# Optimization experiments

Measured on AMD Instinct MI355X. Metric: run time of the kernel, lower is better.

The kernel has to match this reference:

```python
import jax, jax.numpy as jnp
import numpy as np

B, D, NR, H = 8, 64, 6, 3        # batch, input_dim, num_relation, num_hop
R2 = 2 * NR                      # relations incl. inverses
NUM_RULE = R2 ** H               # 1728 combinatorial rules
EPS = 1e-6
TAU = 1.0


def _rule_indices():
    # torch.meshgrid (indexing='ij') over num_hop copies of arange(2*NR), stacked on last dim
    a = np.arange(R2)
    grids = np.meshgrid(*([a] * H), indexing="ij")
    return jnp.asarray(np.stack(grids, -1).reshape(-1, H))  # [NUM_RULE, H] int


def setup_inputs() -> dict:
    key = jax.random.key(0)
    ks = jax.random.split(key, 11)
    s = 0.1
    return {
        "query": jax.random.normal(ks[0], (B, D), jnp.float32),
        "relation_emb": jax.random.normal(ks[1], (R2, D), jnp.float32) * s,      # nn.Embedding(2*NR, D)
        "indicator": jax.random.normal(ks[2], (D,), jnp.float32) * s,            # nn.Embedding(1, D)
        "rel_W": jax.random.normal(ks[3], (H, D, R2 * D), jnp.float32) * s,      # per-layer relation_linear
        "rel_b": jax.random.normal(ks[4], (H, R2 * D), jnp.float32) * s,
        "lin_W": jax.random.normal(ks[5], (H, 13 * D, D), jnp.float32) * s,      # per-layer combine Linear(13D->D)
        "lin_b": jax.random.normal(ks[6], (H, D), jnp.float32) * s,
        "mlp_W1": jax.random.normal(ks[7], (2 * D, D), jnp.float32) * s,
        "mlp_b1": jax.random.normal(ks[8], (D,), jnp.float32) * s,
        "mlp_W2": jax.random.normal(ks[9], (D, 1), jnp.float32) * s,
        "mlp_b2": jax.random.normal(ks[10], (1,), jnp.float32) * s,
    }


def reference(query, relation_emb, indicator, rel_W, rel_b, lin_W, lin_b,
              mlp_W1, mlp_b1, mlp_W2, mlp_b2):
    rel_idx = _rule_indices()                       # [R, H]
    Rn = rel_idx.shape[0]

    # PNA degree scales: each graph is a chain; degree_out+1 (boundary self-message)
    # node 0 -> 1 message (boundary only), nodes 1..H -> 2 messages (edge + boundary)
    log_deg_head = jnp.log(jnp.float32(1.0))
    log_deg_tail = jnp.log(jnp.float32(2.0))
    mean_scale = (log_deg_head + H * log_deg_tail) / (H + 1)
    s_head = log_deg_head / mean_scale
    s_tail = log_deg_tail / mean_scale
    scales_head = jnp.stack([jnp.float32(1.0), s_head, 1.0 / jnp.maximum(s_head, 1e-2)])
    scales_tail = jnp.stack([jnp.float32(1.0), s_tail, 1.0 / jnp.maximum(s_tail, 1e-2)])

    # node-0 PNA update: single message == boundary == indicator (constant across graphs)
    # stats layout per feature dim: (mean, max, min, std)
    f0 = jnp.stack([indicator, indicator, indicator,
                    jnp.full((D,), float(np.sqrt(EPS)), indicator.dtype)], -1).reshape(4 * D)
    upd0 = (f0[:, None] * scales_head).reshape(12 * D)

    # boundary / initial hidden: indicator at node 0 of every graph
    hidden = jnp.zeros((B, Rn, H + 1, D), query.dtype)
    hidden = hidden.at[:, :, 0, :].set(indicator)

    for l in range(H):
        # dependent relation table from the query (relation_linear)
        rel_table = (query @ rel_W[l] + rel_b[l]).reshape(B, R2, D)
        rel = rel_table[:, rel_idx]                 # [B, R, H, D] gather per edge
        msg = hidden[:, :, :-1, :] * rel            # distmult message on edges h -> h+1
        # tail-node PNA stats over message set {msg, boundary=0}
        mean = msg * 0.5
        mx = jnp.maximum(msg, 0.0)
        mn = jnp.minimum(msg, 0.0)
        std = jnp.sqrt(jnp.maximum(msg * msg * 0.25, EPS))   # sq_mean - mean^2 = msg^2/4
        feats = jnp.stack([mean, mx, mn, std], -1).reshape(B, Rn, H, 4 * D)
        upd_tail = (feats[..., None] * scales_tail).reshape(B, Rn, H, 12 * D)
        upd = jnp.concatenate(
            [jnp.broadcast_to(upd0, (B, Rn, 1, 12 * D)), upd_tail], axis=2)
        # combine: relu(Linear(cat([input, update])))
        hidden = jax.nn.relu(
            jnp.concatenate([hidden, upd], -1) @ lin_W[l] + lin_b[l])

    # readout at tail node H, concat per-node query
    feat = jnp.concatenate(
        [hidden[:, :, H, :], jnp.broadcast_to(query[:, None, :], (B, Rn, D))], -1)
    score = (jax.nn.relu(feat @ mlp_W1 + mlp_b1) @ mlp_W2 + mlp_b2)[..., 0]   # [B, R]
    attention = jax.nn.softmax(score / TAU, axis=-1)
    r_emb = relation_emb[rel_idx]                   # [R, H, D]
    subgoals = jnp.einsum("br,rhd->bhd", attention, r_emb)
    masks = jnp.ones((B, H), bool)
    return subgoals, masks
```

## Files before the change

### kernel.cpp

```cpp
#include <hip/hip_runtime.h>
#include <hip/hip_bf16.h>


typedef const float* fp;

#define WS_WT     0
#define WS_RELT   49152
#define WS_QW1    67584
#define WS_Q2     68096
#define WS_QW3    141824
#define WS_SCORES 142592

__device__ __forceinline__ void acc4f(float q, float rv, float4 wv, float& acc){
  float m  = q*rv;
  float am = fabsf(m);
  acc += m  * wv.x;
  acc += am * wv.y;
  acc += fmaxf(am, 2e-3f) * wv.z;
}

__global__ void k_pre1(fp lin_W, fp query, fp rel_W, fp rel_b, fp mlp_W1,
                       fp mlp_b1, float* ws){
  int t = blockIdx.x*256 + threadIdx.x;
  if (t < 49152){
    int c = t & 3; int j = (t>>2)&63; int d = (t>>8)&63; int l = t>>14;
    fp W = lin_W + (size_t)l*832*64 + (64 + 12*d)*64 + j;
    float v = 0.f;
    if (c == 0){
      float w0 = W[0]   + (4.f/3.f)*W[64]  + 0.75f*W[128];
      float w1 = W[192] + (4.f/3.f)*W[256] + 0.75f*W[320];
      float w2 = W[384] + (4.f/3.f)*W[448] + 0.75f*W[512];
      v = 0.5f*w0 + 0.5f*(w1 + w2);
    } else if (c == 1){
      float w1 = W[192] + (4.f/3.f)*W[256] + 0.75f*W[320];
      float w2 = W[384] + (4.f/3.f)*W[448] + 0.75f*W[512];
      v = 0.5f*(w1 - w2);
    } else if (c == 2){
      v = 0.5f*(W[576] + (4.f/3.f)*W[640] + 0.75f*W[704]);
    }
    ws[WS_WT + t] = v;
  } else if (t < 67584){
    int e = t - 49152;
    int d = e & 63; int j = (e>>6)%12; int b = (e/768)&7; int l = e/6144;
    float acc = rel_b[l*768 + j*64 + d];
    fp W = rel_W + (size_t)l*64*768 + j*64 + d;
    fp q = query + b*64;
    #pragma unroll 8
    for (int k=0;k<64;k++) acc += q[k] * W[k*768];
    ws[WS_RELT + e] = acc;
  } else if (t < 68096){
    int e = t - 67584; int b = e>>6; int j = e&63;
    float acc = mlp_b1[j];
    fp q = query + b*64;
    #pragma unroll 8
    for (int i=0;i<64;i++) acc += q[i] * mlp_W1[(64+i)*64 + j];
    ws[WS_QW1 + e] = acc;
  }
}

__global__ void k_mid(fp indicator, fp lin_W, fp lin_b, float* ws){
  __shared__ float sC2[64], sC2W[64], sP1[64], sQ3[12][64];
  int tid = threadIdx.x;
  int w = tid>>6, j = tid&63;
  bool isQ2 = blockIdx.x < 96;
  int b  = isQ2 ? blockIdx.x/12 : blockIdx.x-96;
  int i0 = isQ2 ? blockIdx.x%12 : 0;
  if (w == 0){
    float acc = lin_b[j];
    #pragma unroll 8
    for (int d=0; d<64; d++) acc += 2e-3f * ws[WS_WT + ((d<<6)+j)*4 + 2];
    sC2[j] = fmaxf(acc, 0.f);
  } else if (w == 1 && isQ2){
    const float4* W4 = (const float4*)(ws + WS_WT);
    const float* rel = ws + WS_RELT + (b*12+i0)*64;
    float acc = lin_b[j];
    #pragma unroll 4
    for (int d=0; d<64; d++) acc4f(indicator[d], rel[d], W4[(d<<6)+j], acc);
    sP1[j] = fmaxf(acc, 0.f);
  }
  __syncthreads();
  if (w == 0){
    float a2 = lin_b[64+j];
    fp W1 = lin_W + 832*64;
    #pragma unroll 8
    for (int k=0;k<64;k++) a2 += sC2[k] * W1[k*64+j];
    sC2W[j] = a2;
  }
  __syncthreads();
  const float4* W4 = (const float4*)(ws + WS_WT + 16384);
  const float* rel = ws + WS_RELT + 6144 + (b*12+w)*64;
  if (isQ2){
    float acc = sC2W[j];
    #pragma unroll 4
    for (int d=0; d<64; d++) acc4f(sP1[d], rel[d], W4[(d<<6)+j], acc);
    ws[WS_Q2 + ((b*12+i0)*12+w)*64 + j] = fmaxf(acc, 0.f);
  } else {
    float acc = sC2W[j];
    #pragma unroll 4
    for (int d=0; d<64; d++) acc4f(sC2[d], rel[d], W4[(d<<6)+j], acc);
    sQ3[w][j] = fmaxf(acc, 0.f);
    __syncthreads();
    fp W2 = lin_W + 2*832*64;
    float a = lin_b[128+j];
    #pragma unroll 8
    for (int k=0;k<64;k++) a += sQ3[w][k]*W2[k*64+j];
    ws[WS_QW3 + (b*12+w)*64 + j] = a;
  }
}

__global__ __launch_bounds__(256) void k_score(fp mlp_W1, fp mlp_W2, float* ws){
  __shared__ float wt_s[4096];
  __shared__ float fin[4][4][64];
  int tid = threadIdx.x, w = tid>>6, j = tid&63;
  int wave = blockIdx.x*4 + w;
  int b = blockIdx.x/108;
  int rem = wave%432;
  int i0 = rem/36; int t36 = rem%36;
  int i2 = t36/3;  int i1b = (t36%3)*4;
  const float4* relv = (const float4*)(ws + WS_RELT + 12288 + (b*12+i2)*64);
  const float* q2base = ws + WS_Q2 + ((b*12+i0)*12 + i1b)*64;
  const float4* q0v = (const float4*)(q2base);
  const float4* q1v = (const float4*)(q2base + 64);
  const float4* q2v = (const float4*)(q2base + 128);
  const float4* q3v = (const float4*)(q2base + 192);
  float a0 = ws[WS_QW3 + (b*12+i2)*64 + j];
  float acc0=a0, acc1=a0, acc2=a0, acc3=a0;
  const float4* Wt2 = (const float4*)(ws + WS_WT + 32768);
  for (int ch=0; ch<4; ch++){
    __syncthreads();
    {
      const float4* src = Wt2 + ch*1024;
      float4* dst = (float4*)wt_s;
      #pragma unroll
      for (int k=0; k<4; k++) dst[tid + k*256] = src[tid + k*256];
    }
    __syncthreads();
    #pragma unroll
    for (int dq=0; dq<4; dq++){
      int dc = ch*4 + dq;
      float4 rv = relv[dc];
      float4 qa = q0v[dc], qb = q1v[dc], qc = q2v[dc], qd = q3v[dc];
      const float4* wl = (const float4*)wt_s + dq*256 + j;
      float4 w0 = wl[0], w1 = wl[64], w2 = wl[128], w3 = wl[192];
      acc4f(qa.x, rv.x, w0, acc0); acc4f(qb.x, rv.x, w0, acc1);
      acc4f(qc.x, rv.x, w0, acc2); acc4f(qd.x, rv.x, w0, acc3);
      acc4f(qa.y, rv.y, w1, acc0); acc4f(qb.y, rv.y, w1, acc1);
      acc4f(qc.y, rv.y, w1, acc2); acc4f(qd.y, rv.y, w1, acc3);
      acc4f(qa.z, rv.z, w2, acc0); acc4f(qb.z, rv.z, w2, acc1);
      acc4f(qc.z, rv.z, w2, acc2); acc4f(qd.z, rv.z, w2, acc3);
      acc4f(qa.w, rv.w, w3, acc0); acc4f(qb.w, rv.w, w3, acc1);
      acc4f(qc.w, rv.w, w3, acc2); acc4f(qd.w, rv.w, w3, acc3);
    }
  }
  __syncthreads();
  fin[w][0][j]=fmaxf(acc0,0.f); fin[w][1][j]=fmaxf(acc1,0.f);
  fin[w][2][j]=fmaxf(acc2,0.f); fin[w][3][j]=fmaxf(acc3,0.f);
  __syncthreads();
  float qw = ws[WS_QW1 + b*64 + j];
  float w2v = mlp_W2[j];
  float h0=qw, h1=qw, h2=qw, h3=qw;
  #pragma unroll 8
  for (int i=0;i<64;i++){
    float wv = mlp_W1[i*64+j];
    h0 += fin[w][0][i]*wv; h1 += fin[w][1][i]*wv;
    h2 += fin[w][2][i]*wv; h3 += fin[w][3][i]*wv;
  }
  float s0=fmaxf(h0,0.f)*w2v, s1=fmaxf(h1,0.f)*w2v;
  float s2=fmaxf(h2,0.f)*w2v, s3=fmaxf(h3,0.f)*w2v;
  #pragma unroll
  for (int off=32; off>0; off>>=1){
    s0 += __shfl_down(s0, off, 64); s1 += __shfl_down(s1, off, 64);
    s2 += __shfl_down(s2, off, 64); s3 += __shfl_down(s3, off, 64);
  }
  if (j == 0){
    int rbase = i0*144 + i1b*12 + i2;
    float* S = ws + WS_SCORES + b*1728 + rbase;
    S[0] = s0; S[12] = s1; S[24] = s2; S[36] = s3;
  }
}

__global__ void k_final(fp relation_emb, float* ws, float* out){
  int b = blockIdx.x, tid = threadIdx.x;
  __shared__ float se[1728];
  __shared__ float red[256];
  __shared__ float pb[36][4];
  __shared__ float bins[36];
  const float* sc = ws + WS_SCORES + b*1728;
  float mx = -1e30f;
  for (int r=tid; r<1728; r+=256){ float v = sc[r]; se[r] = v; mx = fmaxf(mx, v); }
  red[tid] = mx; __syncthreads();
  for (int s=128; s>0; s>>=1){ if (tid<s) red[tid] = fmaxf(red[tid], red[tid+s]); __syncthreads(); }
  mx = red[0]; __syncthreads();
  float ts = 0.f;
  for (int r=tid; r<1728; r+=256){ float e = __expf(se[r]-mx); se[r] = e; ts += e; }
  red[tid] = ts; __syncthreads();
  for (int s=128; s>0; s>>=1){ if (tid<s) red[tid] += red[tid+s]; __syncthreads(); }
  float tot = red[0]; __syncthreads();
  if (tid < 144){
    int bin = tid>>2, q = tid&3;
    int h = bin/12, jj = bin%12;
    float a = 0.f;
    if (h == 0){
      const float* p = se + jj*144 + q*36;
      #pragma unroll 4
      for (int k=0;k<36;k++) a += p[k];
    } else if (h == 1){
      for (int t=q*36; t<q*36+36; t++) a += se[(t/12)*144 + jj*12 + (t%12)];
    } else {
      for (int t=q*36; t<q*36+36; t++) a += se[(t/12)*144 + (t%12)*12 + jj];
    }
    pb[bin][q] = a;
  }
  __syncthreads();
  if (tid < 36) bins[tid] = (pb[tid][0]+pb[tid][1]) + (pb[tid][2]+pb[tid][3]);
  __syncthreads();
  if (tid < 192){
    int h = tid>>6, d = tid&63;
    float acc = 0.f;
    #pragma unroll
    for (int jj=0; jj<12; jj++) acc += bins[h*12+jj] * relation_emb[jj*64+d];
    out[b*192 + tid] = acc/tot;
  }
  if (tid >= 192 && tid < 195){
    out[1536 + b*3 + (tid-192)] = 1.0f;
  }
}

extern "C" void kernel_launch(void* const* d_in, const int* in_sizes, int n_in,
                              void* d_out, int out_size, void* d_ws, size_t ws_size,
                              hipStream_t stream){
  fp query        = (fp)d_in[0];
  fp relation_emb = (fp)d_in[1];
  fp indicator    = (fp)d_in[2];
  fp rel_W        = (fp)d_in[3];
  fp rel_b        = (fp)d_in[4];
  fp lin_W        = (fp)d_in[5];
  fp lin_b        = (fp)d_in[6];
  fp mlp_W1       = (fp)d_in[7];
  fp mlp_b1       = (fp)d_in[8];
  fp mlp_W2       = (fp)d_in[9];
  float* ws = (float*)d_ws;
  float* out = (float*)d_out;

  k_pre1 <<<266, 256, 0, stream>>>(lin_W, query, rel_W, rel_b, mlp_W1, mlp_b1, ws);
  k_mid  <<<104, 768, 0, stream>>>(indicator, lin_W, lin_b, ws);
  k_score<<<864, 256, 0, stream>>>(mlp_W1, mlp_W2, ws);
  k_final<<<8,   256, 0, stream>>>(relation_emb, ws, out);
}
```

Measured before the change: 119.4 us.

## Precompute message products and clamps in shared memory, use wave-shuffle softmax reductions

The per-element products q*rel and their clamped absolute values are now computed once into shared memory instead of being recomputed inside every weight-accumulation loop in k_mid and k_score. The inner loops then read float4 vectors of the precomputed values. The k_final max and sum reductions switch from a shared-memory tree to wave shuffles, and several loop unroll factors are raised. This trims ALU work and barrier count in exchange for extra shared memory, an extra sync in k_mid, and more LDS reads in k_score.

```diff
diff --git a/kernel.cpp b/kernel.cpp
--- a/kernel.cpp
+++ b/kernel.cpp
@@ -11,12 +11,13 @@
 #define WS_QW3    141824
 #define WS_SCORES 142592
 
-__device__ __forceinline__ void acc4f(float q, float rv, float4 wv, float& acc){
-  float m  = q*rv;
-  float am = fabsf(m);
-  acc += m  * wv.x;
-  acc += am * wv.y;
-  acc += fmaxf(am, 2e-3f) * wv.z;
+__device__ __forceinline__ void accq(float4 mv, float4 tv,
+                                     float4 wa, float4 wb, float4 wc, float4 wd,
+                                     float& acc){
+  acc += mv.x*wa.x; acc += fabsf(mv.x)*wa.y; acc += tv.x*wa.z;
+  acc += mv.y*wb.x; acc += fabsf(mv.y)*wb.y; acc += tv.y*wb.z;
+  acc += mv.z*wc.x; acc += fabsf(mv.z)*wc.y; acc += tv.z*wc.z;
+  acc += mv.w*wd.x; acc += fabsf(mv.w)*wd.y; acc += tv.w*wd.z;
 }
 
 __global__ void k_pre1(fp lin_W, fp query, fp rel_W, fp rel_b, fp mlp_W1,
@@ -45,14 +46,14 @@
     float acc = rel_b[l*768 + j*64 + d];
     fp W = rel_W + (size_t)l*64*768 + j*64 + d;
     fp q = query + b*64;
-    #pragma unroll 8
+    #pragma unroll 32
     for (int k=0;k<64;k++) acc += q[k] * W[k*768];
     ws[WS_RELT + e] = acc;
   } else if (t < 68096){
     int e = t - 67584; int b = e>>6; int j = e&63;
     float acc = mlp_b1[j];
     fp q = query + b*64;
-    #pragma unroll 8
+    #pragma unroll 32
     for (int i=0;i<64;i++) acc += q[i] * mlp_W1[(64+i)*64 + j];
     ws[WS_QW1 + e] = acc;
   }
@@ -60,6 +61,8 @@
 
 __global__ void k_mid(fp indicator, fp lin_W, fp lin_b, float* ws){
   __shared__ float sC2[64], sC2W[64], sP1[64], sQ3[12][64];
+  __shared__ __align__(16) float mP[64], tP[64];
+  __shared__ __align__(16) float mL[12][64], tL[12][64];
   int tid = threadIdx.x;
   int w = tid>>6, j = tid&63;
   bool isQ2 = blockIdx.x < 96;
@@ -71,38 +74,54 @@
     for (int d=0; d<64; d++) acc += 2e-3f * ws[WS_WT + ((d<<6)+j)*4 + 2];
     sC2[j] = fmaxf(acc, 0.f);
   } else if (w == 1 && isQ2){
-    const float4* W4 = (const float4*)(ws + WS_WT);
     const float* rel = ws + WS_RELT + (b*12+i0)*64;
-    float acc = lin_b[j];
-    #pragma unroll 4
-    for (int d=0; d<64; d++) acc4f(indicator[d], rel[d], W4[(d<<6)+j], acc);
-    sP1[j] = fmaxf(acc, 0.f);
+    float m = indicator[j] * rel[j];
+    mP[j] = m; tP[j] = fmaxf(fabsf(m), 2e-3f);
   }
   __syncthreads();
   if (w == 0){
     float a2 = lin_b[64+j];
     fp W1 = lin_W + 832*64;
-    #pragma unroll 8
+    #pragma unroll 16
     for (int k=0;k<64;k++) a2 += sC2[k] * W1[k*64+j];
     sC2W[j] = a2;
+  } else if (w == 1 && isQ2){
+    const float4* W4 = (const float4*)(ws + WS_WT);
+    float acc = lin_b[j];
+    #pragma unroll
+    for (int dq=0; dq<16; dq++){
+      float4 mv = ((const float4*)mP)[dq], tv = ((const float4*)tP)[dq];
+      float4 wa = W4[(dq*4+0)*64+j], wb = W4[(dq*4+1)*64+j],
+             wc = W4[(dq*4+2)*64+j], wd = W4[(dq*4+3)*64+j];
+      accq(mv,tv,wa,wb,wc,wd,acc);
+    }
+    sP1[j] = fmaxf(acc, 0.f);
+  }
+  __syncthreads();
+  {
+    const float* rel = ws + WS_RELT + 6144 + (b*12+w)*64;
+    float s = isQ2 ? sP1[j] : sC2[j];
+    float m = s * rel[j];
+    mL[w][j] = m; tL[w][j] = fmaxf(fabsf(m), 2e-3f);
   }
   __syncthreads();
   const float4* W4 = (const float4*)(ws + WS_WT + 16384);
-  const float* rel = ws + WS_RELT + 6144 + (b*12+w)*64;
+  float acc = sC2W[j];
+  #pragma unroll
+  for (int dq=0; dq<16; dq++){
+    float4 mv = ((const float4*)mL[w])[dq], tv = ((const float4*)tL[w])[dq];
+    float4 wa = W4[(dq*4+0)*64+j], wb = W4[(dq*4+1)*64+j],
+           wc = W4[(dq*4+2)*64+j], wd = W4[(dq*4+3)*64+j];
+    accq(mv,tv,wa,wb,wc,wd,acc);
+  }
   if (isQ2){
-    float acc = sC2W[j];
-    #pragma unroll 4
-    for (int d=0; d<64; d++) acc4f(sP1[d], rel[d], W4[(d<<6)+j], acc);
     ws[WS_Q2 + ((b*12+i0)*12+w)*64 + j] = fmaxf(acc, 0.f);
   } else {
-    float acc = sC2W[j];
-    #pragma unroll 4
-    for (int d=0; d<64; d++) acc4f(sC2[d], rel[d], W4[(d<<6)+j], acc);
     sQ3[w][j] = fmaxf(acc, 0.f);
     __syncthreads();
     fp W2 = lin_W + 2*832*64;
     float a = lin_b[128+j];
-    #pragma unroll 8
+    #pragma unroll 16
     for (int k=0;k<64;k++) a += sQ3[w][k]*W2[k*64+j];
     ws[WS_QW3 + (b*12+w)*64 + j] = a;
   }
@@ -111,20 +130,26 @@
 __global__ __launch_bounds__(256) void k_score(fp mlp_W1, fp mlp_W2, float* ws){
   __shared__ float wt_s[4096];
   __shared__ float fin[4][4][64];
+  __shared__ __align__(16) float m_s[4][4][64];
+  __shared__ __align__(16) float t_s[4][4][64];
   int tid = threadIdx.x, w = tid>>6, j = tid&63;
   int wave = blockIdx.x*4 + w;
   int b = blockIdx.x/108;
   int rem = wave%432;
   int i0 = rem/36; int t36 = rem%36;
   int i2 = t36/3;  int i1b = (t36%3)*4;
-  const float4* relv = (const float4*)(ws + WS_RELT + 12288 + (b*12+i2)*64);
-  const float* q2base = ws + WS_Q2 + ((b*12+i0)*12 + i1b)*64;
-  const float4* q0v = (const float4*)(q2base);
-  const float4* q1v = (const float4*)(q2base + 64);
-  const float4* q2v = (const float4*)(q2base + 128);
-  const float4* q3v = (const float4*)(q2base + 192);
+  {
+    float rl = ws[WS_RELT + 12288 + (b*12+i2)*64 + j];
+    #pragma unroll
+    for (int r=0;r<4;r++){
+      float qv = ws[WS_Q2 + ((b*12+i0)*12 + i1b + r)*64 + j];
+      float m = qv*rl;
+      m_s[w][r][j] = m;
+      t_s[w][r][j] = fmaxf(fabsf(m), 2e-3f);
+    }
+  }
   float a0 = ws[WS_QW3 + (b*12+i2)*64 + j];
-  float acc0=a0, acc1=a0, acc2=a0, acc3=a0;
+  float acc[4] = {a0, a0, a0, a0};
   const float4* Wt2 = (const float4*)(ws + WS_WT + 32768);
   for (int ch=0; ch<4; ch++){
     __syncthreads();
@@ -138,23 +163,19 @@
     #pragma unroll
     for (int dq=0; dq<4; dq++){
       int dc = ch*4 + dq;
-      float4 rv = relv[dc];
-      float4 qa = q0v[dc], qb = q1v[dc], qc = q2v[dc], qd = q3v[dc];
       const float4* wl = (const float4*)wt_s + dq*256 + j;
-      float4 w0 = wl[0], w1 = wl[64], w2 = wl[128], w3 = wl[192];
-      acc4f(qa.x, rv.x, w0, acc0); acc4f(qb.x, rv.x, w0, acc1);
-      acc4f(qc.x, rv.x, w0, acc2); acc4f(qd.x, rv.x, w0, acc3);
-      acc4f(qa.y, rv.y, w1, acc0); acc4f(qb.y, rv.y, w1, acc1);
-      acc4f(qc.y, rv.y, w1, acc2); acc4f(qd.y, rv.y, w1, acc3);
-      acc4f(qa.z, rv.z, w2, acc0); acc4f(qb.z, rv.z, w2, acc1);
-      acc4f(qc.z, rv.z, w2, acc2); acc4f(qd.z, rv.z, w2, acc3);
-      acc4f(qa.w, rv.w, w3, acc0); acc4f(qb.w, rv.w, w3, acc1);
-      acc4f(qc.w, rv.w, w3, acc2); acc4f(qd.w, rv.w, w3, acc3);
-    }
-  }
-  __syncthreads();
-  fin[w][0][j]=fmaxf(acc0,0.f); fin[w][1][j]=fmaxf(acc1,0.f);
-  fin[w][2][j]=fmaxf(acc2,0.f); fin[w][3][j]=fmaxf(acc3,0.f);
+      float4 wa = wl[0], wb = wl[64], wc = wl[128], wd = wl[192];
+      #pragma unroll
+      for (int r=0;r<4;r++){
+        float4 mv = ((const float4*)m_s[w][r])[dc];
+        float4 tv = ((const float4*)t_s[w][r])[dc];
+        accq(mv,tv,wa,wb,wc,wd,acc[r]);
+      }
+    }
+  }
+  __syncthreads();
+  fin[w][0][j]=fmaxf(acc[0],0.f); fin[w][1][j]=fmaxf(acc[1],0.f);
+  fin[w][2][j]=fmaxf(acc[2],0.f); fin[w][3][j]=fmaxf(acc[3],0.f);
   __syncthreads();
   float qw = ws[WS_QW1 + b*64 + j];
   float w2v = mlp_W2[j];
@@ -181,21 +202,27 @@
 
 __global__ void k_final(fp relation_emb, float* ws, float* out){
   int b = blockIdx.x, tid = threadIdx.x;
+  int w = tid>>6, lane = tid&63;
   __shared__ float se[1728];
-  __shared__ float red[256];
+  __shared__ float wred[4];
   __shared__ float pb[36][4];
   __shared__ float bins[36];
   const float* sc = ws + WS_SCORES + b*1728;
   float mx = -1e30f;
   for (int r=tid; r<1728; r+=256){ float v = sc[r]; se[r] = v; mx = fmaxf(mx, v); }
-  red[tid] = mx; __syncthreads();
-  for (int s=128; s>0; s>>=1){ if (tid<s) red[tid] = fmaxf(red[tid], red[tid+s]); __syncthreads(); }
-  mx = red[0]; __syncthreads();
+  #pragma unroll
+  for (int off=32; off>0; off>>=1) mx = fmaxf(mx, __shfl_xor(mx, off, 64));
+  if (lane == 0) wred[w] = mx;
+  __syncthreads();
+  mx = fmaxf(fmaxf(wred[0],wred[1]), fmaxf(wred[2],wred[3]));
+  __syncthreads();
   float ts = 0.f;
   for (int r=tid; r<1728; r+=256){ float e = __expf(se[r]-mx); se[r] = e; ts += e; }
-  red[tid] = ts; __syncthreads();
-  for (int s=128; s>0; s>>=1){ if (tid<s) red[tid] += red[tid+s]; __syncthreads(); }
-  float tot = red[0]; __syncthreads();
+  #pragma unroll
+  for (int off=32; off>0; off>>=1) ts += __shfl_xor(ts, off, 64);
+  if (lane == 0) wred[w] = ts;
+  __syncthreads();
+  float tot = (wred[0]+wred[1]) + (wred[2]+wred[3]);
   if (tid < 144){
     int bin = tid>>2, q = tid&3;
     int h = bin/12, jj = bin%12;
```

Result: faster. 115.5 us (-3.2%).
